# Kernel tuning notes

Hardware: AMD Instinct MI355X
Metric: run time of the kernel (lower is better)

Reference implementation:

```python
import jax, jax.numpy as jnp
import numpy as np

N_NODES = 100000
INPUT_DIM = 512
OUTPUT_DIM = 128
N_EDGES = 300000


def setup_inputs() -> dict:
    key = jax.random.key(0)
    k1, k2, k3, k4, k5 = jax.random.split(key, 5)
    x = jax.random.normal(k1, (N_NODES, INPUT_DIM), dtype=jnp.float32)
    train_edges = jax.random.randint(k2, (N_EDGES, 2), 0, N_NODES, dtype=jnp.int64)
    train_false_edges = jax.random.randint(k3, (N_EDGES, 2), 0, N_NODES, dtype=jnp.int64)
    # learned params (xavier / kaiming init approximated with uniform fan-based scales)
    limit_w = float(np.sqrt(6.0 / (INPUT_DIM + OUTPUT_DIM)))
    weight = jax.random.uniform(k4, (INPUT_DIM, OUTPUT_DIM), dtype=jnp.float32,
                                minval=-limit_w, maxval=limit_w)
    limit_w3 = float(np.sqrt(6.0 / OUTPUT_DIM) / np.sqrt(2.0))
    weight_three = jax.random.uniform(k5, (OUTPUT_DIM, 1), dtype=jnp.float32,
                                      minval=-limit_w3, maxval=limit_w3)
    return {"x": x, "train_edges": train_edges, "train_false_edges": train_false_edges,
            "weight": weight, "weight_three": weight_three}


def _decode(z, edges, weight_three):
    # gather endpoints, elementwise multiply, matvec against weight_three
    prod = z[edges[:, 0]] * z[edges[:, 1]]  # [E, output_dim]
    return prod @ weight_three               # [E, 1]


def reference(x, train_edges, train_false_edges, weight, weight_three):
    z = x @ weight  # encode: [N, output_dim]
    z1 = _decode(z, train_edges, weight_three)
    z2 = _decode(z, train_false_edges, weight_three)
    return jax.nn.sigmoid(jnp.concatenate((z1, z2), axis=0))
```

## Files before the change

### kernel.cpp

```cpp
#include <hip/hip_runtime.h>
#include <math.h>

#define IN_DIM 512
#define OUT_DIM 128
#define BM 64

typedef __attribute__((ext_vector_type(8))) __bf16 bf16x8;
typedef __attribute__((ext_vector_type(2))) __bf16 bf16x2;
typedef __attribute__((ext_vector_type(4))) float f32x4;
typedef __attribute__((ext_vector_type(2))) float f32x2;

__device__ inline unsigned short f2bf(float f) {
    unsigned u = __float_as_uint(f);
    u += 0x7FFFu + ((u >> 16) & 1u);
    return (unsigned short)(u >> 16);
}
__device__ inline unsigned pack2f(float a, float b) {
    return (unsigned)f2bf(a) | ((unsigned)f2bf(b) << 16);
}

__device__ inline bf16x8 cvt8(const f32x4& lo, const f32x4& hi) {
    bf16x2 p0 = {(__bf16)lo.x, (__bf16)lo.y};
    bf16x2 p1 = {(__bf16)lo.z, (__bf16)lo.w};
    bf16x2 p2 = {(__bf16)hi.x, (__bf16)hi.y};
    bf16x2 p3 = {(__bf16)hi.z, (__bf16)hi.w};
    uint4 u = {__builtin_bit_cast(unsigned, p0), __builtin_bit_cast(unsigned, p1),
               __builtin_bit_cast(unsigned, p2), __builtin_bit_cast(unsigned, p3)};
    return __builtin_bit_cast(bf16x8, u);
}

__device__ inline void gload_lds16(const void* g, void* l) {
    __builtin_amdgcn_global_load_lds(
        (const __attribute__((address_space(1))) void*)g,
        (__attribute__((address_space(3))) void*)l, 16, 0, 0);
}

__global__ void wt2_kernel(const float* __restrict__ w, unsigned short* __restrict__ wt2) {
    int idx = blockIdx.x * 256 + threadIdx.x;
    int k = idx >> 7;
    int n = idx & 127;
    wt2[(((k >> 3) * 128) + n) * 8 + (k & 7)] = f2bf(w[idx]);
}

__global__ __launch_bounds__(512, 8) void gemm_mfma(const float* __restrict__ x,
                                                    const unsigned short* __restrict__ wt2,
                                                    unsigned short* __restrict__ zb,
                                                    int M) {
    __shared__ float sA[8][1024];
    char* const pAb = (char*)sA;

    const int tid  = threadIdx.x;
    const int lane = tid & 63;
    const int wid  = tid >> 6;
    const int wm   = wid >> 1;
    const int wn   = wid & 1;
    const int block_row = blockIdx.x * BM;

    const int fr  = lane & 15;
    const int fk4 = lane >> 4;

    f32x4 acc[4];
#pragma unroll
    for (int j = 0; j < 4; ++j) acc[j] = (f32x4){0.f, 0.f, 0.f, 0.f};

    const int s_cb = ((lane & 7) * 16) ^ ((lane >> 3) << 4);
    int r0 = block_row + wm * 16 + (lane >> 3);     r0 = (r0 < M) ? r0 : (M - 1);
    int r1 = r0 + 8;                                 r1 = (r1 < M) ? r1 : (M - 1);
    const char* sb0 = (const char*)x + (size_t)r0 * 2048 + s_cb;
    const char* sb1 = (const char*)x + (size_t)r1 * 2048 + s_cb;
    char* const wbase = pAb + wid * 4096;

    const int swz = (fr & 7) << 4;
    const int cb0 = (fk4 * 32) ^ swz;
    const int cb1 = (fk4 * 32 + 16) ^ swz;
    const int rb  = fr * 128;

    const unsigned short* pb = wt2 + fk4 * 1024 + (wn * 64 + fr) * 8;

    bf16x8 bv0, bv1, bv2, bv3;

#define LOADB(BYTEOFF)                                              \
    bv0 = *(const bf16x8*)(pb + (BYTEOFF) / 2 + 0);                 \
    bv1 = *(const bf16x8*)(pb + (BYTEOFF) / 2 + 128);               \
    bv2 = *(const bf16x8*)(pb + (BYTEOFF) / 2 + 256);               \
    bv3 = *(const bf16x8*)(pb + (BYTEOFF) / 2 + 384);

#define STAGE(T, BUF)                                               \
    gload_lds16(sb0 + (T) * 128, wbase + (BUF) * 2048);             \
    gload_lds16(sb1 + (T) * 128, wbase + (BUF) * 2048 + 1024);

#define WAITN(N)                                                    \
    asm volatile("s_waitcnt vmcnt(" #N ")" ::: "memory");           \
    __builtin_amdgcn_sched_barrier(0);

#define COMP(BUF)                                                                \
    {                                                                            \
        const char* pT = wbase + (BUF) * 2048;                                   \
        f32x4 lo = *(const f32x4*)(pT + rb + cb0);                               \
        f32x4 hi = *(const f32x4*)(pT + rb + cb1);                               \
        bf16x8 af = cvt8(lo, hi);                                                \
        acc[0] = __builtin_amdgcn_mfma_f32_16x16x32_bf16(bv0, af, acc[0], 0, 0, 0); \
        acc[1] = __builtin_amdgcn_mfma_f32_16x16x32_bf16(bv1, af, acc[1], 0, 0, 0); \
        acc[2] = __builtin_amdgcn_mfma_f32_16x16x32_bf16(bv2, af, acc[2], 0, 0, 0); \
        acc[3] = __builtin_amdgcn_mfma_f32_16x16x32_bf16(bv3, af, acc[3], 0, 0, 0); \
    }

    STAGE(0, 0);

#pragma unroll
    for (int p = 0; p < 8; ++p) {
        LOADB(p * 16384);
        STAGE(2 * p + 1, 1);
        WAITN(2);
        COMP(0);

        LOADB(p * 16384 + 8192);
        if (p < 7) {
            STAGE(2 * p + 2, 0);
            WAITN(2);
        } else {
            WAITN(0);
        }
        COMP(1);
    }

#undef LOADB
#undef STAGE
#undef WAITN
#undef COMP

    const int cm  = lane & 15;
    const int cn0 = (lane >> 4) * 4;
    const int grow = block_row + wm * 16 + cm;
    if (grow < M) {
        unsigned short* zr = zb + (size_t)grow * OUT_DIM + wn * 64 + cn0;
#pragma unroll
        for (int nf = 0; nf < 4; ++nf) {
            uint2 u;
            u.x = pack2f(acc[nf][0], acc[nf][1]);
            u.y = pack2f(acc[nf][2], acc[nf][3]);
            *(uint2*)(zr + nf * 16) = u;
        }
    }
}

__device__ inline float dotw3(const uint4& ua, const uint4& ub, const f32x2* w3v) {
    const unsigned pa[4] = {ua.x, ua.y, ua.z, ua.w};
    const unsigned pb[4] = {ub.x, ub.y, ub.z, ub.w};
    f32x2 vv = (f32x2){0.f, 0.f};
#pragma unroll
    for (int i = 0; i < 4; ++i) {
        f32x2 A = (f32x2){__uint_as_float(pa[i] << 16),
                          __uint_as_float(pa[i] & 0xFFFF0000u)};
        f32x2 B = (f32x2){__uint_as_float(pb[i] << 16),
                          __uint_as_float(pb[i] & 0xFFFF0000u)};
        vv += (A * B) * w3v[i];
    }
    return vv.x + vv.y;
}

__global__ __launch_bounds__(256) void decode_kernel(const unsigned short* __restrict__ zb,
                                                     const int* __restrict__ e1,
                                                     const int* __restrict__ e2,
                                                     const float* __restrict__ w3,
                                                     float* __restrict__ out,
                                                     int E1, int E2) {
    const int tid  = threadIdx.x;
    const int lane = tid & 63;
    const int sub  = lane & 15;
    const int sg   = lane >> 4;
    const int Etot = E1 + E2;
    const int nq   = (Etot + 3) >> 2;

    f32x2 w3v[4];
    {
        const float4 wlo = *(const float4*)(w3 + sub * 8);
        const float4 whi = *(const float4*)(w3 + sub * 8 + 4);
        w3v[0] = (f32x2){wlo.x, wlo.y};
        w3v[1] = (f32x2){wlo.z, wlo.w};
        w3v[2] = (f32x2){whi.x, whi.y};
        w3v[3] = (f32x2){whi.z, whi.w};
    }

    const int wave = blockIdx.x * 4 + (tid >> 6);
    const int S    = gridDim.x * 4;

    for (int q = wave; q < nq; q += 2 * S) {
        const int q2    = q + S;
        const bool has2 = (q2 < nq);

        const int e_a = q * 4 + sg;
        const int e_b = has2 ? (q2 * 4 + sg) : e_a;
        const int ca  = min(e_a, Etot - 1);
        const int cb  = min(e_b, Etot - 1);

        const int2 ia = (ca < E1) ? ((const int2*)e1)[ca] : ((const int2*)e2)[ca - E1];
        const int2 ib = (cb < E1) ? ((const int2*)e1)[cb] : ((const int2*)e2)[cb - E1];

        const uint4 a1 = *(const uint4*)(zb + (size_t)ia.x * OUT_DIM + sub * 8);
        const uint4 b1 = *(const uint4*)(zb + (size_t)ia.y * OUT_DIM + sub * 8);
        const uint4 a2 = *(const uint4*)(zb + (size_t)ib.x * OUT_DIM + sub * 8);
        const uint4 b2 = *(const uint4*)(zb + (size_t)ib.y * OUT_DIM + sub * 8);

        float v1 = dotw3(a1, b1, w3v);
        float v2 = dotw3(a2, b2, w3v);

        v1 += __shfl_xor(v1, 8);  v2 += __shfl_xor(v2, 8);
        v1 += __shfl_xor(v1, 4);  v2 += __shfl_xor(v2, 4);
        v1 += __shfl_xor(v1, 2);  v2 += __shfl_xor(v2, 2);
        v1 += __shfl_xor(v1, 1);  v2 += __shfl_xor(v2, 1);

        if (sub == 0) {
            if (e_a < Etot) out[e_a] = 1.f / (1.f + __expf(-v1));
            if (has2 && e_b < Etot) out[e_b] = 1.f / (1.f + __expf(-v2));
        }
    }
}

extern "C" void kernel_launch(void* const* d_in, const int* in_sizes, int n_in,
                              void* d_out, int out_size, void* d_ws, size_t ws_size,
                              hipStream_t stream) {
    const float* x  = (const float*)d_in[0];
    const int*   e1 = (const int*)d_in[1];
    const int*   e2 = (const int*)d_in[2];
    const float* w  = (const float*)d_in[3];
    const float* w3 = (const float*)d_in[4];

    float* out = (float*)d_out;

    const int M  = in_sizes[0] / IN_DIM;
    const int E1 = in_sizes[1] / 2;
    const int E2 = in_sizes[2] / 2;

    unsigned short* zbuf = (unsigned short*)d_ws;
    unsigned short* wt2  = zbuf + (size_t)M * OUT_DIM;

    wt2_kernel<<<(IN_DIM * OUT_DIM) / 256, 256, 0, stream>>>(w, wt2);
    gemm_mfma<<<(M + BM - 1) / BM, 512, 0, stream>>>(x, wt2, zbuf, M);
    decode_kernel<<<2048, 256, 0, stream>>>(zbuf, e1, e2, w3, out, E1, E2);
}
```

Before: 102.9 us.

## Restructure GEMM to 4-wave blocks with 2x4 MFMA tiles and shared double buffer

The encode GEMM goes from 8 waves per block, each with a private LDS slice and 16 rows, to 4 waves per block that share a double-buffered 64x32 fp32 tile and each compute 32 rows. Each wave now reuses every B fragment across two A fragments, halving B loads from global per MFMA. The per-wave vmcnt-based pipelining is replaced by a block-wide __syncthreads per K step, which adds barrier stalls. Launch bounds change to 256 threads with 6 blocks per CU.

After: 89.31 us. 13.2% less time.

```diff
diff --git a/kernel.cpp b/kernel.cpp
--- a/kernel.cpp
+++ b/kernel.cpp
@@ -4,6 +4,8 @@
 #define IN_DIM 512
 #define OUT_DIM 128
 #define BM 64
+#define BK 32
+#define NKT (IN_DIM / BK)
 
 typedef __attribute__((ext_vector_type(8))) __bf16 bf16x8;
 typedef __attribute__((ext_vector_type(2))) __bf16 bf16x2;
@@ -42,11 +44,11 @@
     wt2[(((k >> 3) * 128) + n) * 8 + (k & 7)] = f2bf(w[idx]);
 }
 
-__global__ __launch_bounds__(512, 8) void gemm_mfma(const float* __restrict__ x,
+__global__ __launch_bounds__(256, 6) void gemm_mfma(const float* __restrict__ x,
                                                     const unsigned short* __restrict__ wt2,
                                                     unsigned short* __restrict__ zb,
                                                     int M) {
-    __shared__ float sA[8][1024];
+    __shared__ float sA[2][BM * BK];
     char* const pAb = (char*)sA;
 
     const int tid  = threadIdx.x;
@@ -59,87 +61,86 @@
     const int fr  = lane & 15;
     const int fk4 = lane >> 4;
 
-    f32x4 acc[4];
-#pragma unroll
-    for (int j = 0; j < 4; ++j) acc[j] = (f32x4){0.f, 0.f, 0.f, 0.f};
+    f32x4 acc[2][4];
+#pragma unroll
+    for (int i = 0; i < 2; ++i)
+#pragma unroll
+        for (int j = 0; j < 4; ++j) acc[i][j] = (f32x4){0.f, 0.f, 0.f, 0.f};
 
     const int s_cb = ((lane & 7) * 16) ^ ((lane >> 3) << 4);
-    int r0 = block_row + wm * 16 + (lane >> 3);     r0 = (r0 < M) ? r0 : (M - 1);
-    int r1 = r0 + 8;                                 r1 = (r1 < M) ? r1 : (M - 1);
-    const char* sb0 = (const char*)x + (size_t)r0 * 2048 + s_cb;
-    const char* sb1 = (const char*)x + (size_t)r1 * 2048 + s_cb;
-    char* const wbase = pAb + wid * 4096;
-
-    const int swz = (fr & 7) << 4;
-    const int cb0 = (fk4 * 32) ^ swz;
-    const int cb1 = (fk4 * 32 + 16) ^ swz;
-    const int rb  = fr * 128;
+    const char* sb0;
+    const char* sb1;
+    {
+        int r0 = block_row + (wid * 2 + 0) * 8 + (lane >> 3); r0 = (r0 < M) ? r0 : (M - 1);
+        int r1 = block_row + (wid * 2 + 1) * 8 + (lane >> 3); r1 = (r1 < M) ? r1 : (M - 1);
+        sb0 = (const char*)x + (size_t)r0 * 2048 + s_cb;
+        sb1 = (const char*)x + (size_t)r1 * 2048 + s_cb;
+    }
+    const int d0 = (wid * 2 + 0) * 1024;
+    const int d1 = (wid * 2 + 1) * 1024;
+
+    const int rowa0 = wm * 32 + fr;
+    const int rowa1 = rowa0 + 16;
+    const int swz   = (fr & 7) << 4;
+    const int c0    = (fk4 * 32) ^ swz;
+    const int c1    = (fk4 * 32 + 16) ^ swz;
 
     const unsigned short* pb = wt2 + fk4 * 1024 + (wn * 64 + fr) * 8;
 
-    bf16x8 bv0, bv1, bv2, bv3;
-
-#define LOADB(BYTEOFF)                                              \
-    bv0 = *(const bf16x8*)(pb + (BYTEOFF) / 2 + 0);                 \
-    bv1 = *(const bf16x8*)(pb + (BYTEOFF) / 2 + 128);               \
-    bv2 = *(const bf16x8*)(pb + (BYTEOFF) / 2 + 256);               \
-    bv3 = *(const bf16x8*)(pb + (BYTEOFF) / 2 + 384);
-
 #define STAGE(T, BUF)                                               \
-    gload_lds16(sb0 + (T) * 128, wbase + (BUF) * 2048);             \
-    gload_lds16(sb1 + (T) * 128, wbase + (BUF) * 2048 + 1024);
-
-#define WAITN(N)                                                    \
-    asm volatile("s_waitcnt vmcnt(" #N ")" ::: "memory");           \
-    __builtin_amdgcn_sched_barrier(0);
-
-#define COMP(BUF)                                                                \
+    gload_lds16(sb0 + (T) * 128, pAb + (BUF) * 8192 + d0);          \
+    gload_lds16(sb1 + (T) * 128, pAb + (BUF) * 8192 + d1);
+
+#define COMP(T, BUF)                                                             \
     {                                                                            \
-        const char* pT = wbase + (BUF) * 2048;                                   \
-        f32x4 lo = *(const f32x4*)(pT + rb + cb0);                               \
-        f32x4 hi = *(const f32x4*)(pT + rb + cb1);                               \
-        bf16x8 af = cvt8(lo, hi);                                                \
-        acc[0] = __builtin_amdgcn_mfma_f32_16x16x32_bf16(bv0, af, acc[0], 0, 0, 0); \
-        acc[1] = __builtin_amdgcn_mfma_f32_16x16x32_bf16(bv1, af, acc[1], 0, 0, 0); \
-        acc[2] = __builtin_amdgcn_mfma_f32_16x16x32_bf16(bv2, af, acc[2], 0, 0, 0); \
-        acc[3] = __builtin_amdgcn_mfma_f32_16x16x32_bf16(bv3, af, acc[3], 0, 0, 0); \
+        const char* pT = pAb + (BUF) * 8192;                                     \
+        f32x4 lo0 = *(const f32x4*)(pT + rowa0 * 128 + c0);                      \
+        f32x4 hi0 = *(const f32x4*)(pT + rowa0 * 128 + c1);                      \
+        f32x4 lo1 = *(const f32x4*)(pT + rowa1 * 128 + c0);                      \
+        f32x4 hi1 = *(const f32x4*)(pT + rowa1 * 128 + c1);                      \
+        bf16x8 af0 = cvt8(lo0, hi0);                                             \
+        bf16x8 af1 = cvt8(lo1, hi1);                                             \
+        bf16x8 bv0 = *(const bf16x8*)(pb + (T) * 4096 + 0);                      \
+        bf16x8 bv1 = *(const bf16x8*)(pb + (T) * 4096 + 128);                    \
+        bf16x8 bv2 = *(const bf16x8*)(pb + (T) * 4096 + 256);                    \
+        bf16x8 bv3 = *(const bf16x8*)(pb + (T) * 4096 + 384);                    \
+        acc[0][0] = __builtin_amdgcn_mfma_f32_16x16x32_bf16(bv0, af0, acc[0][0], 0, 0, 0); \
+        acc[0][1] = __builtin_amdgcn_mfma_f32_16x16x32_bf16(bv1, af0, acc[0][1], 0, 0, 0); \
+        acc[0][2] = __builtin_amdgcn_mfma_f32_16x16x32_bf16(bv2, af0, acc[0][2], 0, 0, 0); \
+        acc[0][3] = __builtin_amdgcn_mfma_f32_16x16x32_bf16(bv3, af0, acc[0][3], 0, 0, 0); \
+        acc[1][0] = __builtin_amdgcn_mfma_f32_16x16x32_bf16(bv0, af1, acc[1][0], 0, 0, 0); \
+        acc[1][1] = __builtin_amdgcn_mfma_f32_16x16x32_bf16(bv1, af1, acc[1][1], 0, 0, 0); \
+        acc[1][2] = __builtin_amdgcn_mfma_f32_16x16x32_bf16(bv2, af1, acc[1][2], 0, 0, 0); \
+        acc[1][3] = __builtin_amdgcn_mfma_f32_16x16x32_bf16(bv3, af1, acc[1][3], 0, 0, 0); \
     }
 
     STAGE(0, 0);
-
-#pragma unroll
-    for (int p = 0; p < 8; ++p) {
-        LOADB(p * 16384);
-        STAGE(2 * p + 1, 1);
-        WAITN(2);
-        COMP(0);
-
-        LOADB(p * 16384 + 8192);
-        if (p < 7) {
-            STAGE(2 * p + 2, 0);
-            WAITN(2);
-        } else {
-            WAITN(0);
-        }
-        COMP(1);
-    }
-
-#undef LOADB
+    __syncthreads();
+
+#pragma unroll
+    for (int t = 0; t < NKT; ++t) {
+        if (t + 1 < NKT) STAGE(t + 1, (t + 1) & 1);
+        COMP(t, t & 1);
+        __syncthreads();
+    }
+
 #undef STAGE
-#undef WAITN
 #undef COMP
 
     const int cm  = lane & 15;
     const int cn0 = (lane >> 4) * 4;
-    const int grow = block_row + wm * 16 + cm;
-    if (grow < M) {
-        unsigned short* zr = zb + (size_t)grow * OUT_DIM + wn * 64 + cn0;
-#pragma unroll
-        for (int nf = 0; nf < 4; ++nf) {
-            uint2 u;
-            u.x = pack2f(acc[nf][0], acc[nf][1]);
-            u.y = pack2f(acc[nf][2], acc[nf][3]);
-            *(uint2*)(zr + nf * 16) = u;
+#pragma unroll
+    for (int mf = 0; mf < 2; ++mf) {
+        const int grow = block_row + wm * 32 + mf * 16 + cm;
+        if (grow < M) {
+            unsigned short* zr = zb + (size_t)grow * OUT_DIM + wn * 64 + cn0;
+#pragma unroll
+            for (int nf = 0; nf < 4; ++nf) {
+                uint2 u;
+                u.x = pack2f(acc[mf][nf][0], acc[mf][nf][1]);
+                u.y = pack2f(acc[mf][nf][2], acc[mf][nf][3]);
+                *(uint2*)(zr + nf * 16) = u;
+            }
         }
     }
 }
@@ -236,6 +237,6 @@
     unsigned short* wt2  = zbuf + (size_t)M * OUT_DIM;
 
     wt2_kernel<<<(IN_DIM * OUT_DIM) / 256, 256, 0, stream>>>(w, wt2);
-    gemm_mfma<<<(M + BM - 1) / BM, 512, 0, stream>>>(x, wt2, zbuf, M);
+    gemm_mfma<<<(M + BM - 1) / BM, 256, 0, stream>>>(x, wt2, zbuf, M);
     decode_kernel<<<2048, 256, 0, stream>>>(zbuf, e1, e2, w3, out, E1, E2);
 }
```
